# Kernel tuning notes

Hardware: AMD Instinct MI355X
Metric: run time of the kernel (lower is better)

The kernel has to match this reference:

```python
import jax, jax.numpy as jnp
import numpy as np

N_NODES = 50000
N_EDGES = 800000
ATOM_F = 64
NBR_F = 64
EPS = 1e-5


def batch_norm(x, gamma, beta):
    # BatchNorm1d in training mode: batch stats, biased variance
    mu = x.mean(axis=0)
    var = x.var(axis=0)
    return gamma * (x - mu) * jax.lax.rsqrt(var + EPS) + beta


def setup_inputs() -> dict:
    key = jax.random.key(0)
    ks = jax.random.split(key, 8)
    d_in = 2 * ATOM_F + NBR_F  # 192
    d_out = 2 * ATOM_F         # 128
    return {
        "atom_in_fea": jax.random.normal(ks[0], (N_NODES, ATOM_F), dtype=jnp.float32),
        "nbr_fea": jax.random.normal(ks[1], (N_EDGES, NBR_F), dtype=jnp.float32),
        "edge_src": jax.random.randint(ks[2], (N_EDGES,), 0, N_NODES),
        "edge_dst": jax.random.randint(ks[3], (N_EDGES,), 0, N_NODES),
        "W_full": jax.random.normal(ks[4], (d_in, d_out), dtype=jnp.float32) / np.sqrt(d_in),
        "b_full": jnp.zeros((d_out,), dtype=jnp.float32),
        "bn1_g": jnp.ones((d_out,), dtype=jnp.float32),
        "bn1_b": jnp.zeros((d_out,), dtype=jnp.float32),
        "bn2_g": jnp.ones((ATOM_F,), dtype=jnp.float32),
        "bn2_b": jnp.zeros((ATOM_F,), dtype=jnp.float32),
    }


def reference(atom_in_fea, nbr_fea, edge_src, edge_dst,
              W_full, b_full, bn1_g, bn1_b, bn2_g, bn2_b):
    # gather endpoint features per edge: [E, 2*A + Nf]
    atom_src = atom_in_fea[edge_src]
    atom_dst = atom_in_fea[edge_dst]
    total = jnp.concatenate([atom_src, atom_dst, nbr_fea], axis=1)
    total = batch_norm(total @ W_full + b_full, bn1_g, bn1_b)  # [E, 2*A]
    filter_fea, core_fea = jnp.split(total, 2, axis=1)
    nbr_msg = jax.nn.sigmoid(filter_fea) * jax.nn.softplus(core_fea)  # [E, A]
    # scatter-add messages back to destination nodes
    atom_update = jax.ops.segment_sum(nbr_msg, edge_dst, num_segments=atom_in_fea.shape[0])
    return jax.nn.softplus(atom_in_fea + batch_norm(atom_update, bn2_g, bn2_b))
```

## Files before the change

kernel.cpp:

```cpp
#include <hip/hip_runtime.h>
#include <hip/hip_fp16.h>
#include <math.h>

#define N_NODES 50000
#define N_EDGES 800000
#define ATOMF 64
#define DIN 192
#define DOUT 128
#define EPB 64
#define NTILES (N_EDGES / EPB)
#define LDW 200
#define NSLOT (EPB * 25)

typedef __attribute__((ext_vector_type(8))) short bf16x8;
typedef __attribute__((ext_vector_type(8))) short s16x8;
typedef __attribute__((ext_vector_type(4))) float f32x4;

__device__ __forceinline__ short f2bf(float f) {
  unsigned u = __float_as_uint(f);
  u += 0x7fffu + ((u >> 16) & 1u);
  return (short)(u >> 16);
}
__device__ __forceinline__ float bf2f(unsigned short u) {
  return __uint_as_float(((unsigned)u) << 16);
}
__device__ __forceinline__ unsigned short f2h(float f) {
  __half h = __float2half_rn(f);
  return *(unsigned short*)&h;
}
__device__ __forceinline__ float h2f(unsigned short u) {
  __half h = *(__half*)&u;
  return __half2float(h);
}
__device__ __forceinline__ float softplus_f(float x) {
  return fmaxf(x, 0.f) + log1pf(__expf(-fabsf(x)));
}
__device__ __forceinline__ float sigmoid_f(float x) {
  return 1.f / (1.f + __expf(-x));
}
__device__ __forceinline__ float fast_sigmoid(float x) {
  return __builtin_amdgcn_rcpf(1.f + __expf(-x));
}
__device__ __forceinline__ float fast_softplus(float x) {
  return fmaxf(x, 0.f) + __logf(1.f + __expf(-fabsf(x)));
}

#define GLOAD16(g, l)                                                          \
  __builtin_amdgcn_global_load_lds(                                            \
      (const __attribute__((address_space(1))) void*)(g),                      \
      (__attribute__((address_space(3))) void*)(l), 16, 0, 0)

__launch_bounds__(256)
__global__ void precvt_k(const float* __restrict__ atom,
                         const float* __restrict__ nbr,
                         const int* __restrict__ edst,
                         unsigned short* __restrict__ atom_bf,
                         unsigned short* __restrict__ nbr_bf,
                         int* __restrict__ deg) {
  const int NA = N_NODES * ATOMF / 8;
  const int NB = N_EDGES * ATOMF / 8;
  int gid = blockIdx.x * blockDim.x + threadIdx.x;
  int stride = gridDim.x * blockDim.x;
  if (deg) {
    for (int i = gid; i < N_EDGES; i += stride) atomicAdd(&deg[edst[i]], 1);
  }
  for (int i = gid; i < NA + NB; i += stride) {
    const float* s;
    unsigned short* d;
    if (i < NA) { s = atom + (size_t)i * 8; d = atom_bf + (size_t)i * 8; }
    else        { s = nbr + (size_t)(i - NA) * 8; d = nbr_bf + (size_t)(i - NA) * 8; }
    float4 a = ((const float4*)s)[0];
    float4 b = ((const float4*)s)[1];
    s16x8 t;
    t[0] = f2bf(a.x); t[1] = f2bf(a.y); t[2] = f2bf(a.z); t[3] = f2bf(a.w);
    t[4] = f2bf(b.x); t[5] = f2bf(b.y); t[6] = f2bf(b.z); t[7] = f2bf(b.w);
    *(s16x8*)d = t;
  }
}

__launch_bounds__(1024)
__global__ void scan_k(const int* __restrict__ deg,
                       int* __restrict__ rowptr,
                       int* __restrict__ cursor) {
  __shared__ int wsum[16];
  const int tid = threadIdx.x;
  const int lane = tid & 63, wv = tid >> 6;
  const int N4 = N_NODES / 4;
  int base = 0;
  for (int c0 = 0; c0 < N4; c0 += 1024) {
    int i4 = c0 + tid;
    int4 v = make_int4(0, 0, 0, 0);
    if (i4 < N4) v = ((const int4*)deg)[i4];
    int t = v.x + v.y + v.z + v.w;
    int s = t;
    #pragma unroll
    for (int d = 1; d < 64; d <<= 1) {
      int u = __shfl_up(s, d, 64);
      if (lane >= d) s += u;
    }
    if (lane == 63) wsum[wv] = s;
    __syncthreads();
    if (wv == 0 && lane < 16) {
      int ws = wsum[lane];
      #pragma unroll
      for (int d = 1; d < 16; d <<= 1) {
        int u = __shfl_up(ws, d, 64);
        if (lane >= d) ws += u;
      }
      wsum[lane] = ws;
    }
    __syncthreads();
    int wbase = wv ? wsum[wv - 1] : 0;
    int excl = base + wbase + s - t;
    if (i4 < N4) {
      int4 r;
      r.x = excl;
      r.y = excl + v.x;
      r.z = r.y + v.y;
      r.w = r.z + v.z;
      ((int4*)rowptr)[i4] = r;
      ((int4*)cursor)[i4] = r;
    }
    int tot = wsum[15];
    __syncthreads();
    base += tot;
  }
  if (tid == 0) rowptr[N_NODES] = base;
}

__launch_bounds__(256)
__global__ void fill_k(const int* __restrict__ edst,
                       int* __restrict__ cursor,
                       int* __restrict__ iperm) {
  int gid = blockIdx.x * 256 + threadIdx.x;
  if (gid < N_EDGES) {
    int pos = atomicAdd(&cursor[edst[gid]], 1);
    iperm[gid] = pos;
  }
}

__device__ __forceinline__ void stage_tile(const unsigned short* __restrict__ atom_bf,
                                           const unsigned short* __restrict__ nbr_bf,
                                           const int* __restrict__ esrc,
                                           const int* __restrict__ edst,
                                           int e0, unsigned short* lbase,
                                           const int* g_enc, int wv) {
  #pragma unroll
  for (int it = 0; it < 7; ++it) {
    if (it * 256 + wv * 64 < NSLOT) {
      int e = g_enc[it];
      int row = e & 255;
      int coff = (e >> 8) & 255;
      int sel = e >> 16;
      const unsigned short* src;
      if (sel < 2) {
        const int* ip = sel ? edst : esrc;
        int idx = ip[e0 + row];
        src = atom_bf + (size_t)idx * ATOMF + coff;
      } else {
        src = nbr_bf + (size_t)(e0 + row) * ATOMF + coff;
      }
      GLOAD16(src, lbase + (size_t)(it * 256 + wv * 64) * 8);
    }
  }
}

__launch_bounds__(256, 4)
__global__ void edge_gemm(const unsigned short* __restrict__ atom_bf,
                          const unsigned short* __restrict__ nbr_bf,
                          const int* __restrict__ esrc,
                          const int* __restrict__ edst,
                          const float* __restrict__ W,
                          float* __restrict__ stats,
                          unsigned short* __restrict__ zt) {
  __shared__ unsigned short Tl[EPB * LDW];

  const int tid = threadIdx.x;
  const int lane = tid & 63;
  const int wv = tid >> 6;
  const int l15 = lane & 15;
  const int lg = lane >> 4;
  const int colF = wv * 16 + l15;
  const int colC = colF + 64;

  bf16x8 wf[2][6];
  #pragma unroll
  for (int cg = 0; cg < 2; ++cg) {
    #pragma unroll
    for (int kk = 0; kk < 6; ++kk) {
      bf16x8 t;
      #pragma unroll
      for (int jj = 0; jj < 8; ++jj)
        t[jj] = f2bf(W[(size_t)(kk * 32 + lg * 8 + jj) * 128 + cg * 64 + colF]);
      wf[cg][kk] = t;
    }
  }

  int g_enc[7];
  #pragma unroll
  for (int it = 0; it < 7; ++it) {
    int s = it * 256 + tid;
    if (s >= NSLOT) s = 0;
    int row = s / 25;
    int w = s - row * 25;
    int sel, coff;
    if (w < 8)       { sel = 0; coff = w * 8; }
    else if (w < 16) { sel = 1; coff = (w - 8) * 8; }
    else             { sel = 2; coff = (w < 24 ? (w - 16) * 8 : 0); }
    g_enc[it] = row | (coff << 8) | (sel << 16);
  }

  float fs[2] = {0.f, 0.f}, fq[2] = {0.f, 0.f};

  for (int tile = blockIdx.x; tile < NTILES; tile += gridDim.x) {
    stage_tile(atom_bf, nbr_bf, esrc, edst, tile * EPB, Tl, g_enc, wv);
    __syncthreads();

    f32x4 acc[2][4] = {};
    #pragma unroll
    for (int rg = 0; rg < 4; ++rg) {
      #pragma unroll
      for (int kk = 0; kk < 6; ++kk) {
        bf16x8 a = *(const bf16x8*)&Tl[(rg * 16 + l15) * LDW + kk * 32 + lg * 8];
        acc[0][rg] = __builtin_amdgcn_mfma_f32_16x16x32_bf16(a, wf[0][kk], acc[0][rg], 0, 0, 0);
        acc[1][rg] = __builtin_amdgcn_mfma_f32_16x16x32_bf16(a, wf[1][kk], acc[1][rg], 0, 0, 0);
      }
    }

    #pragma unroll
    for (int cg = 0; cg < 2; ++cg) {
      unsigned short* zb = zt + ((size_t)tile * 128 + cg * 64 + colF) * 64 + lg * 4;
      #pragma unroll
      for (int rg = 0; rg < 4; ++rg) {
        float z0 = acc[cg][rg][0], z1 = acc[cg][rg][1];
        float z2 = acc[cg][rg][2], z3 = acc[cg][rg][3];
        fs[cg] += (z0 + z1) + (z2 + z3);
        fq[cg] += z0 * z0 + z1 * z1 + z2 * z2 + z3 * z3;
        uint2 p;
        p.x = (unsigned)f2h(z0) | ((unsigned)f2h(z1) << 16);
        p.y = (unsigned)f2h(z2) | ((unsigned)f2h(z3) << 16);
        *(uint2*)(zb + rg * 16) = p;
      }
    }
    __syncthreads();
  }

  #pragma unroll
  for (int cg = 0; cg < 2; ++cg) {
    fs[cg] += __shfl_xor(fs[cg], 16, 64); fs[cg] += __shfl_xor(fs[cg], 32, 64);
    fq[cg] += __shfl_xor(fq[cg], 16, 64); fq[cg] += __shfl_xor(fq[cg], 32, 64);
  }
  if (lane < 16) {
    atomicAdd(&stats[colF], fs[0]);
    atomicAdd(&stats[colC], fs[1]);
    atomicAdd(&stats[128 + colF], fq[0]);
    atomicAdd(&stats[128 + colC], fq[1]);
  }
}

__global__ void finalize1_k(const float* __restrict__ stats,
                            const float* __restrict__ g,
                            const float* __restrict__ be,
                            float* __restrict__ ab) {
  int n = threadIdx.x;
  float mu = stats[n] * (1.f / N_EDGES);
  float var = stats[128 + n] * (1.f / N_EDGES) - mu * mu;
  float a = g[n] * rsqrtf(var + 1e-5f);
  ab[n] = a;
  ab[128 + n] = be[n] - mu * a;
}

__launch_bounds__(256)
__global__ void msg_k(const unsigned short* __restrict__ zt,
                      const float* __restrict__ ab,
                      const int* __restrict__ iperm,
                      unsigned short* __restrict__ msg) {
  __shared__ unsigned short ml[64][72];
  const int tile = blockIdx.x;
  const int tid = threadIdx.x;
  const int c = tid & 63;
  const int rg = tid >> 6;
  const unsigned short* fb = zt + ((size_t)tile * 128 + c) * 64 + rg * 16;
  const unsigned short* gb = fb + (size_t)64 * 64;
  s16x8 f0 = *(const s16x8*)fb;
  s16x8 f1 = *(const s16x8*)(fb + 8);
  s16x8 g0 = *(const s16x8*)gb;
  s16x8 g1 = *(const s16x8*)(gb + 8);
  float af = ab[c], cf = ab[128 + c];
  float ag = ab[64 + c], cg = ab[192 + c];
  #pragma unroll
  for (int k = 0; k < 16; ++k) {
    unsigned short fu = (unsigned short)(k < 8 ? f0[k] : f1[k - 8]);
    unsigned short gu = (unsigned short)(k < 8 ? g0[k] : g1[k - 8]);
    float f = af * h2f(fu) + cf;
    float g = ag * h2f(gu) + cg;
    ml[rg * 16 + k][c] = f2h(fast_sigmoid(f) * fast_softplus(g));
  }
  const int r = tid >> 2;
  const int pos = iperm[tile * 64 + r];
  __syncthreads();
  const int cq = (tid & 3) * 16;
  s16x8 o0, o1;
  #pragma unroll
  for (int k = 0; k < 8; ++k) { o0[k] = ml[r][cq + k]; o1[k] = ml[r][cq + 8 + k]; }
  unsigned short* ob = msg + (size_t)pos * 64 + cq;
  *(s16x8*)ob = o0;
  *(s16x8*)(ob + 8) = o1;
}

__launch_bounds__(256)
__global__ void gather_k(const unsigned short* __restrict__ msg,
                         const int* __restrict__ rowptr,
                         float* __restrict__ out) {
  int n = blockIdx.x * 4 + (threadIdx.x >> 6);
  if (n >= N_NODES) return;
  int lane = threadIdx.x & 63;
  int g = lane >> 3;
  int q = lane & 7;
  int s = rowptr[n], e = rowptr[n + 1];
  float acc[8] = {0.f, 0.f, 0.f, 0.f, 0.f, 0.f, 0.f, 0.f};
  for (int i = s + g; i < e; i += 8) {
    s16x8 v = *(const s16x8*)(msg + (size_t)i * 64 + q * 8);
    #pragma unroll
    for (int k = 0; k < 8; ++k) acc[k] += h2f((unsigned short)v[k]);
  }
  #pragma unroll
  for (int k = 0; k < 8; ++k) {
    acc[k] += __shfl_xor(acc[k], 8, 64);
    acc[k] += __shfl_xor(acc[k], 16, 64);
    acc[k] += __shfl_xor(acc[k], 32, 64);
  }
  if (g == 0) {
    float4 a = make_float4(acc[0], acc[1], acc[2], acc[3]);
    float4 b = make_float4(acc[4], acc[5], acc[6], acc[7]);
    float4* ob = (float4*)(out + (size_t)n * 64 + q * 8);
    ob[0] = a; ob[1] = b;
  }
}

__launch_bounds__(256)
__global__ void stats2_k(const float* __restrict__ upd, float* __restrict__ stats2) {
  int tid = threadIdx.x;
  int gid = blockIdx.x * 256 + tid;
  int stride = gridDim.x * 256;
  float4 s = make_float4(0.f, 0.f, 0.f, 0.f);
  float4 q = make_float4(0.f, 0.f, 0.f, 0.f);
  for (int i = gid; i < N_NODES * 16; i += stride) {
    float4 v = ((const float4*)upd)[i];
    s.x += v.x; s.y += v.y; s.z += v.z; s.w += v.w;
    q.x += v.x * v.x; q.y += v.y * v.y; q.z += v.z * v.z; q.w += v.w * v.w;
  }
  int lane = tid & 63;
  int wv = tid >> 6;
  s.x += __shfl_xor(s.x, 16, 64); s.x += __shfl_xor(s.x, 32, 64);
  s.y += __shfl_xor(s.y, 16, 64); s.y += __shfl_xor(s.y, 32, 64);
  s.z += __shfl_xor(s.z, 16, 64); s.z += __shfl_xor(s.z, 32, 64);
  s.w += __shfl_xor(s.w, 16, 64); s.w += __shfl_xor(s.w, 32, 64);
  q.x += __shfl_xor(q.x, 16, 64); q.x += __shfl_xor(q.x, 32, 64);
  q.y += __shfl_xor(q.y, 16, 64); q.y += __shfl_xor(q.y, 32, 64);
  q.z += __shfl_xor(q.z, 16, 64); q.z += __shfl_xor(q.z, 32, 64);
  q.w += __shfl_xor(q.w, 16, 64); q.w += __shfl_xor(q.w, 32, 64);
  __shared__ float red[4 * 128];
  if (lane < 16) {
    int f = lane * 4;
    red[wv * 128 + f + 0] = s.x; red[wv * 128 + f + 1] = s.y;
    red[wv * 128 + f + 2] = s.z; red[wv * 128 + f + 3] = s.w;
    red[wv * 128 + 64 + f + 0] = q.x; red[wv * 128 + 64 + f + 1] = q.y;
    red[wv * 128 + 64 + f + 2] = q.z; red[wv * 128 + 64 + f + 3] = q.w;
  }
  __syncthreads();
  if (tid < 128) {
    float v = red[tid] + red[128 + tid] + red[256 + tid] + red[384 + tid];
    atomicAdd(&stats2[tid], v);
  }
}

__global__ void finalize2_k(const float* __restrict__ stats2,
                            const float* __restrict__ g,
                            const float* __restrict__ be,
                            float* __restrict__ ab2) {
  int f = threadIdx.x;
  float mu = stats2[f] * (1.f / N_NODES);
  float var = stats2[64 + f] * (1.f / N_NODES) - mu * mu;
  float a = g[f] * rsqrtf(var + 1e-5f);
  ab2[f] = a;
  ab2[64 + f] = be[f] - mu * a;
}

__launch_bounds__(256)
__global__ void out_k(const float* __restrict__ atom,
                      const float* __restrict__ ab2,
                      float* __restrict__ out) {
  int gid = blockIdx.x * 256 + threadIdx.x;
  int stride = gridDim.x * 256;
  for (int i = gid; i < N_NODES * 16; i += stride) {
    float4 u = ((const float4*)out)[i];
    float4 x = ((const float4*)atom)[i];
    int f = (i & 15) * 4;
    float4 r;
    r.x = softplus_f(x.x + u.x * ab2[f + 0] + ab2[64 + f + 0]);
    r.y = softplus_f(x.y + u.y * ab2[f + 1] + ab2[64 + f + 1]);
    r.z = softplus_f(x.z + u.z * ab2[f + 2] + ab2[64 + f + 2]);
    r.w = softplus_f(x.w + u.w * ab2[f + 3] + ab2[64 + f + 3]);
    ((float4*)out)[i] = r;
  }
}

__launch_bounds__(256)
__global__ void scatter_k(const unsigned short* __restrict__ zt,
                          const int* __restrict__ edst,
                          const float* __restrict__ ab,
                          float* __restrict__ out) {
  int gid = blockIdx.x * 256 + threadIdx.x;
  int r8 = gid & 7;
  int c = (gid >> 3) & 63;
  int tile = gid >> 9;
  const unsigned short* fb = zt + ((size_t)tile * 128 + c) * 64 + r8 * 8;
  const unsigned short* gb = fb + 64 * 64;
  s16x8 f8 = *(const s16x8*)fb;
  s16x8 g8 = *(const s16x8*)gb;
  float af = ab[c], cf = ab[128 + c];
  float ag = ab[64 + c], cg = ab[192 + c];
  int4 d0 = *(const int4*)(edst + tile * 64 + r8 * 8);
  int4 d1 = *(const int4*)(edst + tile * 64 + r8 * 8 + 4);
  int dsts[8] = {d0.x, d0.y, d0.z, d0.w, d1.x, d1.y, d1.z, d1.w};
  #pragma unroll
  for (int i = 0; i < 8; ++i) {
    float f = af * h2f((unsigned short)f8[i]) + cf;
    float g = ag * h2f((unsigned short)g8[i]) + cg;
    float m = sigmoid_f(f) * softplus_f(g);
    atomicAdd(out + (size_t)dsts[i] * ATOMF + c, m);
  }
}

template<int PASS>
__launch_bounds__(256, 2)
__global__ void edge_pass(const float* __restrict__ atom,
                          const float* __restrict__ nbr,
                          const int* __restrict__ esrc,
                          const int* __restrict__ edst,
                          const float* __restrict__ W,
                          const float* __restrict__ bvec,
                          float* __restrict__ stats,
                          const float* __restrict__ ab,
                          float* __restrict__ upd) {
  __shared__ short Wl[DOUT * LDW];
  __shared__ short Tl[EPB * LDW];
  __shared__ int eix[2 * EPB];

  const int tid = threadIdx.x;
  const int lane = tid & 63;
  const int wv = tid >> 6;
  const int l15 = lane & 15;
  const int lg = lane >> 4;

  for (int i = tid; i < DIN * DOUT; i += 256) {
    int k = i >> 7, n = i & 127;
    Wl[n * LDW + k] = f2bf(W[i]);
  }
  float bcol[8], acol[8], ccol[8];
  #pragma unroll
  for (int j = 0; j < 8; ++j) {
    int n = j * 16 + l15;
    bcol[j] = bvec[n];
    if constexpr (PASS == 1) { acol[j] = ab[n]; ccol[j] = ab[DOUT + n]; }
    else { acol[j] = 0.f; ccol[j] = 0.f; }
  }
  float fsum[8], fsq[8];
  #pragma unroll
  for (int j = 0; j < 8; ++j) { fsum[j] = 0.f; fsq[j] = 0.f; }

  for (int tile = blockIdx.x; tile < NTILES; tile += gridDim.x) {
    const int e0 = tile * EPB;
    __syncthreads();
    if (tid < EPB) eix[tid] = esrc[e0 + tid];
    else if (tid < 2 * EPB) eix[tid] = edst[e0 + tid - EPB];
    __syncthreads();
    for (int i = tid; i < EPB * 96; i += 256) {
      int row = i / 96;
      int cl = (i - row * 96) * 2;
      const float* p;
      if (cl < 64)       p = atom + (size_t)eix[row] * 64 + cl;
      else if (cl < 128) p = atom + (size_t)eix[EPB + row] * 64 + (cl - 64);
      else               p = nbr + (size_t)(e0 + row) * 64 + (cl - 128);
      float2 v = *(const float2*)p;
      unsigned pk = (unsigned)(unsigned short)f2bf(v.x)
                  | ((unsigned)(unsigned short)f2bf(v.y) << 16);
      *(unsigned*)&Tl[row * LDW + cl] = pk;
    }
    __syncthreads();
    f32x4 acc[8] = {};
    const int abase = (wv * 16 + l15) * LDW + lg * 8;
    #pragma unroll
    for (int kk = 0; kk < 6; ++kk) {
      bf16x8 afr = *(const bf16x8*)&Tl[abase + kk * 32];
      #pragma unroll
      for (int j = 0; j < 8; ++j) {
        bf16x8 bfr = *(const bf16x8*)&Wl[(j * 16 + l15) * LDW + lg * 8 + kk * 32];
        acc[j] = __builtin_amdgcn_mfma_f32_16x16x32_bf16(afr, bfr, acc[j], 0, 0, 0);
      }
    }
    if constexpr (PASS == 0) {
      #pragma unroll
      for (int j = 0; j < 8; ++j)
        #pragma unroll
        for (int r = 0; r < 4; ++r) {
          float z = acc[j][r] + bcol[j];
          fsum[j] += z; fsq[j] += z * z;
        }
    } else {
      #pragma unroll
      for (int r = 0; r < 4; ++r) {
        int row = wv * 16 + lg * 4 + r;
        int d = eix[EPB + row];
        float* urow = upd + (size_t)d * 64;
        #pragma unroll
        for (int j = 0; j < 4; ++j) {
          float f = (acc[j][r] + bcol[j]) * acol[j] + ccol[j];
          float g = (acc[j + 4][r] + bcol[j + 4]) * acol[j + 4] + ccol[j + 4];
          atomicAdd(&urow[j * 16 + l15], sigmoid_f(f) * softplus_f(g));
        }
      }
    }
  }
  if constexpr (PASS == 0) {
    #pragma unroll
    for (int j = 0; j < 8; ++j) {
      fsum[j] += __shfl_xor(fsum[j], 16, 64);
      fsum[j] += __shfl_xor(fsum[j], 32, 64);
      fsq[j]  += __shfl_xor(fsq[j], 16, 64);
      fsq[j]  += __shfl_xor(fsq[j], 32, 64);
    }
    __syncthreads();
    float* redf = (float*)Tl;
    if (lane < 16) {
      #pragma unroll
      for (int j = 0; j < 8; ++j) {
        redf[wv * 256 + j * 16 + lane] = fsum[j];
        redf[wv * 256 + 128 + j * 16 + lane] = fsq[j];
      }
    }
    __syncthreads();
    float s = redf[tid] + redf[256 + tid] + redf[512 + tid] + redf[768 + tid];
    atomicAdd(&stats[tid], s);
  }
}

extern "C" void kernel_launch(void* const* d_in, const int* in_sizes, int n_in,
                              void* d_out, int out_size, void* d_ws, size_t ws_size,
                              hipStream_t stream) {
  const float* atom = (const float*)d_in[0];
  const float* nbr  = (const float*)d_in[1];
  const int*   esrc = (const int*)d_in[2];
  const int*   edst = (const int*)d_in[3];
  const float* W    = (const float*)d_in[4];
  const float* bvec = (const float*)d_in[5];
  const float* g1   = (const float*)d_in[6];
  const float* b1   = (const float*)d_in[7];
  const float* g2   = (const float*)d_in[8];
  const float* b2   = (const float*)d_in[9];
  float* out = (float*)d_out;
  char* ws = (char*)d_ws;

  float* stats1 = (float*)ws;
  float* ab1    = stats1 + 256;
  float* stats2 = stats1 + 512;
  float* ab2    = stats1 + 640;

  const size_t OFF_ATOM = 4096;
  const size_t SZ_ATOM  = (size_t)N_NODES * ATOMF * 2;
  const size_t OFF_NBR  = OFF_ATOM + SZ_ATOM;
  const size_t SZ_NBR   = (size_t)N_EDGES * ATOMF * 2;
  const size_t OFF_ZT   = OFF_NBR + SZ_NBR;
  const size_t SZ_ZT    = (size_t)N_EDGES * DOUT * 2;
  const size_t NEED_OLD = OFF_ZT + SZ_ZT;
  const size_t OFF_PERM = NEED_OLD;
  const size_t SZ_PERM  = (size_t)N_EDGES * 4;
  const size_t OFF_DEG  = OFF_PERM + SZ_PERM;
  const size_t OFF_RP   = OFF_DEG + N_NODES * 4;
  const size_t OFF_CUR  = OFF_RP + (N_NODES + 1) * 4 + 12;
  const size_t NEED_NEW = OFF_CUR + N_NODES * 4;

  hipMemsetAsync(stats1, 0, 768 * sizeof(float), stream);

  if (ws_size >= NEED_NEW) {
    unsigned short* atom_bf = (unsigned short*)(ws + OFF_ATOM);
    unsigned short* nbr_bf  = (unsigned short*)(ws + OFF_NBR);
    unsigned short* zt      = (unsigned short*)(ws + OFF_ZT);
    unsigned short* msg     = nbr_bf;
    int* iperm  = (int*)(ws + OFF_PERM);
    int* deg    = (int*)(ws + OFF_DEG);
    int* rowptr = (int*)(ws + OFF_RP);
    int* cursor = (int*)(ws + OFF_CUR);

    hipMemsetAsync(deg, 0, N_NODES * sizeof(int), stream);
    precvt_k<<<2048, 256, 0, stream>>>(atom, nbr, edst, atom_bf, nbr_bf, deg);
    scan_k<<<1, 1024, 0, stream>>>(deg, rowptr, cursor);
    fill_k<<<(N_EDGES + 255) / 256, 256, 0, stream>>>(edst, cursor, iperm);

    edge_gemm<<<1536, 256, 0, stream>>>(atom_bf, nbr_bf, esrc, edst, W, stats1, zt);
    finalize1_k<<<1, 128, 0, stream>>>(stats1, g1, b1, ab1);

    msg_k<<<NTILES, 256, 0, stream>>>(zt, ab1, iperm, msg);
    gather_k<<<(N_NODES + 3) / 4, 256, 0, stream>>>(msg, rowptr, out);
  } else if (ws_size >= NEED_OLD) {
    unsigned short* atom_bf = (unsigned short*)(ws + OFF_ATOM);
    unsigned short* nbr_bf  = (unsigned short*)(ws + OFF_NBR);
    unsigned short* zt      = (unsigned short*)(ws + OFF_ZT);
    hipMemsetAsync(out, 0, (size_t)N_NODES * 64 * sizeof(float), stream);
    precvt_k<<<2048, 256, 0, stream>>>(atom, nbr, edst, atom_bf, nbr_bf, nullptr);
    edge_gemm<<<1536, 256, 0, stream>>>(atom_bf, nbr_bf, esrc, edst, W, stats1, zt);
    finalize1_k<<<1, 128, 0, stream>>>(stats1, g1, b1, ab1);
    scatter_k<<<25000, 256, 0, stream>>>(zt, edst, ab1, out);
  } else {
    hipMemsetAsync(out, 0, (size_t)N_NODES * 64 * sizeof(float), stream);
    edge_pass<0><<<512, 256, 0, stream>>>(atom, nbr, esrc, edst, W, bvec,
                                          stats1, nullptr, nullptr);
    finalize1_k<<<1, 128, 0, stream>>>(stats1, g1, b1, ab1);
    edge_pass<1><<<512, 256, 0, stream>>>(atom, nbr, esrc, edst, W, bvec,
                                          nullptr, ab1, out);
  }

  stats2_k<<<512, 256, 0, stream>>>(out, stats2);
  finalize2_k<<<1, 64, 0, stream>>>(stats2, g2, b2, ab2);
  out_k<<<512, 256, 0, stream>>>(atom, ab2, out);
}
```

Baseline: 472.1 us.

## Scatter GEMM output in destination-sorted order and fuse message into gather

The edge GEMM now stages each tile's fp16 pre-activations in shared memory and writes full 128-wide rows to their CSR-permuted positions, so the separate message kernel and its intermediate buffer pass are dropped. The gather kernel applies the batch-norm affine, sigmoid and softplus while summing each node's incoming edges, one channel per lane. This removes one full read/write pass over edge data. In exchange the GEMM gains two extra barriers and scattered global writes, its grid shrinks from 1536 to 1024 blocks, and the gather does more math with 2-byte loads per lane and serial per-node loops. The old scatter fallback path is also removed.

```diff
diff --git a/kernel.cpp b/kernel.cpp
--- a/kernel.cpp
+++ b/kernel.cpp
@@ -11,6 +11,7 @@
 #define NTILES (N_EDGES / EPB)
 #define LDW 200
 #define NSLOT (EPB * 25)
+#define ZLD 136
 
 typedef __attribute__((ext_vector_type(8))) short bf16x8;
 typedef __attribute__((ext_vector_type(8))) short s16x8;
@@ -20,9 +21,6 @@
   unsigned u = __float_as_uint(f);
   u += 0x7fffu + ((u >> 16) & 1u);
   return (short)(u >> 16);
-}
-__device__ __forceinline__ float bf2f(unsigned short u) {
-  return __uint_as_float(((unsigned)u) << 16);
 }
 __device__ __forceinline__ unsigned short f2h(float f) {
   __half h = __float2half_rn(f);
@@ -170,9 +168,10 @@
                           const unsigned short* __restrict__ nbr_bf,
                           const int* __restrict__ esrc,
                           const int* __restrict__ edst,
+                          const int* __restrict__ iperm,
                           const float* __restrict__ W,
                           float* __restrict__ stats,
-                          unsigned short* __restrict__ zt) {
+                          unsigned short* __restrict__ zc) {
   __shared__ unsigned short Tl[EPB * LDW];
 
   const int tid = threadIdx.x;
@@ -210,6 +209,9 @@
     g_enc[it] = row | (coff << 8) | (sel << 16);
   }
 
+  const int orow = tid >> 2;
+  const int oq = tid & 3;
+
   float fs[2] = {0.f, 0.f}, fq[2] = {0.f, 0.f};
 
   for (int tile = blockIdx.x; tile < NTILES; tile += gridDim.x) {
@@ -229,19 +231,38 @@
 
     #pragma unroll
     for (int cg = 0; cg < 2; ++cg) {
-      unsigned short* zb = zt + ((size_t)tile * 128 + cg * 64 + colF) * 64 + lg * 4;
       #pragma unroll
       for (int rg = 0; rg < 4; ++rg) {
         float z0 = acc[cg][rg][0], z1 = acc[cg][rg][1];
         float z2 = acc[cg][rg][2], z3 = acc[cg][rg][3];
         fs[cg] += (z0 + z1) + (z2 + z3);
         fq[cg] += z0 * z0 + z1 * z1 + z2 * z2 + z3 * z3;
-        uint2 p;
-        p.x = (unsigned)f2h(z0) | ((unsigned)f2h(z1) << 16);
-        p.y = (unsigned)f2h(z2) | ((unsigned)f2h(z3) << 16);
-        *(uint2*)(zb + rg * 16) = p;
-      }
-    }
+      }
+    }
+
+    __syncthreads();
+
+    #pragma unroll
+    for (int cg = 0; cg < 2; ++cg)
+      #pragma unroll
+      for (int rg = 0; rg < 4; ++rg)
+        #pragma unroll
+        for (int r = 0; r < 4; ++r)
+          Tl[(rg * 16 + lg * 4 + r) * ZLD + cg * 64 + colF] = f2h(acc[cg][rg][r]);
+
+    __syncthreads();
+
+    {
+      int pos = iperm[tile * 64 + orow];
+      const s16x8* src = (const s16x8*)&Tl[orow * ZLD + oq * 32];
+      s16x8 v0 = src[0], v1 = src[1], v2 = src[2], v3 = src[3];
+      unsigned short* dst = zc + (size_t)pos * 128 + oq * 32;
+      *(s16x8*)dst = v0;
+      *(s16x8*)(dst + 8) = v1;
+      *(s16x8*)(dst + 16) = v2;
+      *(s16x8*)(dst + 24) = v3;
+    }
+
     __syncthreads();
   }
 
@@ -271,71 +292,24 @@
 }
 
 __launch_bounds__(256)
-__global__ void msg_k(const unsigned short* __restrict__ zt,
-                      const float* __restrict__ ab,
-                      const int* __restrict__ iperm,
-                      unsigned short* __restrict__ msg) {
-  __shared__ unsigned short ml[64][72];
-  const int tile = blockIdx.x;
-  const int tid = threadIdx.x;
-  const int c = tid & 63;
-  const int rg = tid >> 6;
-  const unsigned short* fb = zt + ((size_t)tile * 128 + c) * 64 + rg * 16;
-  const unsigned short* gb = fb + (size_t)64 * 64;
-  s16x8 f0 = *(const s16x8*)fb;
-  s16x8 f1 = *(const s16x8*)(fb + 8);
-  s16x8 g0 = *(const s16x8*)gb;
-  s16x8 g1 = *(const s16x8*)(gb + 8);
-  float af = ab[c], cf = ab[128 + c];
-  float ag = ab[64 + c], cg = ab[192 + c];
-  #pragma unroll
-  for (int k = 0; k < 16; ++k) {
-    unsigned short fu = (unsigned short)(k < 8 ? f0[k] : f1[k - 8]);
-    unsigned short gu = (unsigned short)(k < 8 ? g0[k] : g1[k - 8]);
-    float f = af * h2f(fu) + cf;
-    float g = ag * h2f(gu) + cg;
-    ml[rg * 16 + k][c] = f2h(fast_sigmoid(f) * fast_softplus(g));
-  }
-  const int r = tid >> 2;
-  const int pos = iperm[tile * 64 + r];
-  __syncthreads();
-  const int cq = (tid & 3) * 16;
-  s16x8 o0, o1;
-  #pragma unroll
-  for (int k = 0; k < 8; ++k) { o0[k] = ml[r][cq + k]; o1[k] = ml[r][cq + 8 + k]; }
-  unsigned short* ob = msg + (size_t)pos * 64 + cq;
-  *(s16x8*)ob = o0;
-  *(s16x8*)(ob + 8) = o1;
-}
-
-__launch_bounds__(256)
-__global__ void gather_k(const unsigned short* __restrict__ msg,
+__global__ void gather_k(const unsigned short* __restrict__ zc,
                          const int* __restrict__ rowptr,
+                         const float* __restrict__ ab,
                          float* __restrict__ out) {
   int n = blockIdx.x * 4 + (threadIdx.x >> 6);
   if (n >= N_NODES) return;
-  int lane = threadIdx.x & 63;
-  int g = lane >> 3;
-  int q = lane & 7;
+  int c = threadIdx.x & 63;
+  float af = ab[c], cf = ab[128 + c];
+  float ag = ab[64 + c], cg2 = ab[192 + c];
   int s = rowptr[n], e = rowptr[n + 1];
-  float acc[8] = {0.f, 0.f, 0.f, 0.f, 0.f, 0.f, 0.f, 0.f};
-  for (int i = s + g; i < e; i += 8) {
-    s16x8 v = *(const s16x8*)(msg + (size_t)i * 64 + q * 8);
-    #pragma unroll
-    for (int k = 0; k < 8; ++k) acc[k] += h2f((unsigned short)v[k]);
-  }
-  #pragma unroll
-  for (int k = 0; k < 8; ++k) {
-    acc[k] += __shfl_xor(acc[k], 8, 64);
-    acc[k] += __shfl_xor(acc[k], 16, 64);
-    acc[k] += __shfl_xor(acc[k], 32, 64);
-  }
-  if (g == 0) {
-    float4 a = make_float4(acc[0], acc[1], acc[2], acc[3]);
-    float4 b = make_float4(acc[4], acc[5], acc[6], acc[7]);
-    float4* ob = (float4*)(out + (size_t)n * 64 + q * 8);
-    ob[0] = a; ob[1] = b;
-  }
+  float acc = 0.f;
+  for (int i = s; i < e; ++i) {
+    const unsigned short* row = zc + (size_t)i * 128;
+    float f = af * h2f(row[c]) + cf;
+    float g = ag * h2f(row[64 + c]) + cg2;
+    acc += fast_sigmoid(f) * fast_softplus(g);
+  }
+  out[(size_t)n * 64 + c] = acc;
 }
 
 __launch_bounds__(256)
@@ -406,33 +380,6 @@
   }
 }
 
-__launch_bounds__(256)
-__global__ void scatter_k(const unsigned short* __restrict__ zt,
-                          const int* __restrict__ edst,
-                          const float* __restrict__ ab,
-                          float* __restrict__ out) {
-  int gid = blockIdx.x * 256 + threadIdx.x;
-  int r8 = gid & 7;
-  int c = (gid >> 3) & 63;
-  int tile = gid >> 9;
-  const unsigned short* fb = zt + ((size_t)tile * 128 + c) * 64 + r8 * 8;
-  const unsigned short* gb = fb + 64 * 64;
-  s16x8 f8 = *(const s16x8*)fb;
-  s16x8 g8 = *(const s16x8*)gb;
-  float af = ab[c], cf = ab[128 + c];
-  float ag = ab[64 + c], cg = ab[192 + c];
-  int4 d0 = *(const int4*)(edst + tile * 64 + r8 * 8);
-  int4 d1 = *(const int4*)(edst + tile * 64 + r8 * 8 + 4);
-  int dsts[8] = {d0.x, d0.y, d0.z, d0.w, d1.x, d1.y, d1.z, d1.w};
-  #pragma unroll
-  for (int i = 0; i < 8; ++i) {
-    float f = af * h2f((unsigned short)f8[i]) + cf;
-    float g = ag * h2f((unsigned short)g8[i]) + cg;
-    float m = sigmoid_f(f) * softplus_f(g);
-    atomicAdd(out + (size_t)dsts[i] * ATOMF + c, m);
-  }
-}
-
 template<int PASS>
 __launch_bounds__(256, 2)
 __global__ void edge_pass(const float* __restrict__ atom,
@@ -573,8 +520,7 @@
   const size_t SZ_NBR   = (size_t)N_EDGES * ATOMF * 2;
   const size_t OFF_ZT   = OFF_NBR + SZ_NBR;
   const size_t SZ_ZT    = (size_t)N_EDGES * DOUT * 2;
-  const size_t NEED_OLD = OFF_ZT + SZ_ZT;
-  const size_t OFF_PERM = NEED_OLD;
+  const size_t OFF_PERM = OFF_ZT + SZ_ZT;
   const size_t SZ_PERM  = (size_t)N_EDGES * 4;
   const size_t OFF_DEG  = OFF_PERM + SZ_PERM;
   const size_t OFF_RP   = OFF_DEG + N_NODES * 4;
@@ -586,8 +532,7 @@
   if (ws_size >= NEED_NEW) {
     unsigned short* atom_bf = (unsigned short*)(ws + OFF_ATOM);
     unsigned short* nbr_bf  = (unsigned short*)(ws + OFF_NBR);
-    unsigned short* zt      = (unsigned short*)(ws + OFF_ZT);
-    unsigned short* msg     = nbr_bf;
+    unsigned short* zc      = (unsigned short*)(ws + OFF_ZT);
     int* iperm  = (int*)(ws + OFF_PERM);
     int* deg    = (int*)(ws + OFF_DEG);
     int* rowptr = (int*)(ws + OFF_RP);
@@ -598,20 +543,11 @@
     scan_k<<<1, 1024, 0, stream>>>(deg, rowptr, cursor);
     fill_k<<<(N_EDGES + 255) / 256, 256, 0, stream>>>(edst, cursor, iperm);
 
-    edge_gemm<<<1536, 256, 0, stream>>>(atom_bf, nbr_bf, esrc, edst, W, stats1, zt);
+    edge_gemm<<<1024, 256, 0, stream>>>(atom_bf, nbr_bf, esrc, edst, iperm,
+                                        W, stats1, zc);
     finalize1_k<<<1, 128, 0, stream>>>(stats1, g1, b1, ab1);
 
-    msg_k<<<NTILES, 256, 0, stream>>>(zt, ab1, iperm, msg);
-    gather_k<<<(N_NODES + 3) / 4, 256, 0, stream>>>(msg, rowptr, out);
-  } else if (ws_size >= NEED_OLD) {
-    unsigned short* atom_bf = (unsigned short*)(ws + OFF_ATOM);
-    unsigned short* nbr_bf  = (unsigned short*)(ws + OFF_NBR);
-    unsigned short* zt      = (unsigned short*)(ws + OFF_ZT);
-    hipMemsetAsync(out, 0, (size_t)N_NODES * 64 * sizeof(float), stream);
-    precvt_k<<<2048, 256, 0, stream>>>(atom, nbr, edst, atom_bf, nbr_bf, nullptr);
-    edge_gemm<<<1536, 256, 0, stream>>>(atom_bf, nbr_bf, esrc, edst, W, stats1, zt);
-    finalize1_k<<<1, 128, 0, stream>>>(stats1, g1, b1, ab1);
-    scatter_k<<<25000, 256, 0, stream>>>(zt, edst, ab1, out);
+    gather_k<<<(N_NODES + 3) / 4, 256, 0, stream>>>(zc, rowptr, ab1, out);
   } else {
     hipMemsetAsync(out, 0, (size_t)N_NODES * 64 * sizeof(float), stream);
     edge_pass<0><<<512, 256, 0, stream>>>(atom, nbr, esrc, edst, W, bvec,
```

After: 452.9 us. 4.1% less time.
